# Performance work log

Measured on AMD Instinct MI355X. Metric: run time of the kernel, lower is better.

The kernel has to match this reference:

```python
import jax, jax.numpy as jnp
import numpy as np

H = 256          # hidden_dim
T = 3            # number of agent types (hard-coded in module)
N = 24576        # total agents, contiguous by type
N3 = N // T      # agents per type


def _ln(x, s, b):
    mu = jnp.mean(x, -1, keepdims=True)
    v = jnp.var(x, -1, keepdims=True)
    return (x - mu) * jax.lax.rsqrt(v + 1e-5) * s + b


def setup_inputs() -> dict:
    key = jax.random.key(0)
    ks = jax.random.split(key, 20)
    def p(i, shape, scale=0.02):
        return jax.random.normal(ks[i], shape, jnp.float32) * scale
    inp = {}
    inp['agent_x'] = p(0, (N, H), 1.0)
    inp['lane_x'] = p(1, (N, H), 1.0)
    inp['poly_x'] = p(2, (N, H), 1.0)
    inp['l2a_src'] = jax.random.randint(ks[3], (N,), 0, N)
    inp['g2a_src'] = jax.random.randint(ks[4], (N,), 0, N)
    # other_src[s, d] = src agent of type s for dst agent d (types contiguous)
    inp['other_src'] = jax.random.randint(ks[5], (T, N), 0, N3) + (jnp.arange(T) * N3)[:, None]
    # per-agent-type params
    inp['self_W'] = p(6, (T, H, H)); inp['self_b'] = jnp.zeros((T, H))
    inp['out_W'] = p(7, (T, 4 * H, H)); inp['out_b'] = jnp.zeros((T, H))
    inp['ffn_ln_s'] = jnp.ones((T, H)); inp['ffn_ln_b'] = jnp.zeros((T, H))
    inp['ffn_w1'] = p(8, (T, H, 4 * H)); inp['ffn_b1'] = jnp.zeros((T, 4 * H))
    inp['ffn_w2'] = p(9, (T, 4 * H, H)); inp['ffn_b2'] = jnp.zeros((T, H))
    inp['ffn_w3'] = p(10, (T, H, 4 * H)); inp['ffn_b3'] = jnp.zeros((T, 4 * H))
    # shared edge MLPs (prenorm: LN -> w1 -> relu -> w2)
    inp['l2a_ln_s'] = jnp.ones((3 * H,)); inp['l2a_ln_b'] = jnp.zeros((3 * H,))
    inp['l2a_w1'] = p(11, (3 * H, 4 * H)); inp['l2a_b1'] = jnp.zeros((4 * H,))
    inp['l2a_w2'] = p(12, (4 * H, H)); inp['l2a_b2'] = jnp.zeros((H,))
    inp['g2a_ln_s'] = jnp.ones((2 * H,)); inp['g2a_ln_b'] = jnp.zeros((2 * H,))
    inp['g2a_w1'] = p(13, (2 * H, 4 * H)); inp['g2a_b1'] = jnp.zeros((4 * H,))
    inp['g2a_w2'] = p(14, (4 * H, H)); inp['g2a_b2'] = jnp.zeros((H,))
    # per-src-agent-type 'other' MLPs
    inp['oth_ln_s'] = jnp.ones((T, 3 * H)); inp['oth_ln_b'] = jnp.zeros((T, 3 * H))
    inp['oth_w1'] = p(15, (T, 3 * H, 4 * H)); inp['oth_b1'] = jnp.zeros((T, 4 * H))
    inp['oth_w2'] = p(16, (T, 4 * H, H)); inp['oth_b2'] = jnp.zeros((T, H))
    return inp


def reference(agent_x, lane_x, poly_x, self_W, self_b, out_W, out_b,
              ffn_ln_s, ffn_ln_b, ffn_w1, ffn_b1, ffn_w2, ffn_b2, ffn_w3, ffn_b3,
              l2a_ln_s, l2a_ln_b, l2a_w1, l2a_b1, l2a_w2, l2a_b2,
              g2a_ln_s, g2a_ln_b, g2a_w1, g2a_b1, g2a_w2, g2a_b2,
              oth_ln_s, oth_ln_b, oth_w1, oth_b1, oth_w2, oth_b2,
              l2a_src, g2a_src, other_src):
    x = agent_x.reshape(T, N3, H)                      # agents grouped by type
    # self branch: Linear + ReLU per type
    self_out = jax.nn.relu(jnp.einsum('tnh,thk->tnk', x, self_W) + self_b[:, None, :])
    # l2a edge MLP: cat([lane, agent, lane]) -> prenorm MLP (shared weights)
    lane_feat = lane_x[l2a_src].reshape(T, N3, H)
    l2a_in = jnp.concatenate([lane_feat, x, lane_feat], -1)      # [T,N3,3H]
    l2a_out = jax.nn.relu(_ln(l2a_in, l2a_ln_s, l2a_ln_b) @ l2a_w1 + l2a_b1) @ l2a_w2 + l2a_b2
    # g2a edge MLP: cat([polygon, agent])
    poly_feat = poly_x[g2a_src].reshape(T, N3, H)
    g2a_in = jnp.concatenate([poly_feat, x], -1)                 # [T,N3,2H]
    g2a_out = jax.nn.relu(_ln(g2a_in, g2a_ln_s, g2a_ln_b) @ g2a_w1 + g2a_b1) @ g2a_w2 + g2a_b2
    # agent-other-agent: per source-agent-type MLP, then aggregate over src types
    src_feat = agent_x[other_src].reshape(T, T, N3, H)           # [src_t, dst_t, N3, H]
    xb = jnp.broadcast_to(x[None], (T, T, N3, H))
    oth_in = jnp.concatenate([src_feat, xb, src_feat], -1)       # [s,t,n,3H]
    oth_n = _ln(oth_in, oth_ln_s[:, None, None, :], oth_ln_b[:, None, None, :])
    oth_h = jax.nn.relu(jnp.einsum('stnd,sdm->stnm', oth_n, oth_w1) + oth_b1[:, None, None, :])
    oth_out = jnp.einsum('stnm,smh->stnh', oth_h, oth_w2) + oth_b2[:, None, None, :]
    other_agg = oth_out.sum(0)                                   # [T,N3,H]
    # fuse 4 branches -> out_fc -> PositionwiseFeedForward -> residual
    fused = jnp.concatenate([self_out, l2a_out, g2a_out, other_agg], -1)  # [T,N3,4H]
    out = jnp.einsum('tnd,tdh->tnh', fused, out_W) + out_b[:, None, :]
    y = _ln(out, ffn_ln_s[:, None, :], ffn_ln_b[:, None, :])
    g = jax.nn.silu(jnp.einsum('tnh,thm->tnm', y, ffn_w1) + ffn_b1[:, None, :])
    u = jnp.einsum('tnh,thm->tnm', y, ffn_w3) + ffn_b3[:, None, :]
    out = out + jnp.einsum('tnm,tmh->tnh', g * u, ffn_w2) + ffn_b2[:, None, :]
    return (out + x).reshape(N, H)
```

## Files before the change

### kernel.cpp

```cpp
#include <hip/hip_runtime.h>
#include <hip/hip_bf16.h>

typedef __hip_bfloat16 bf16;
typedef __bf16 v8bf __attribute__((ext_vector_type(8)));
typedef float f32x4 __attribute__((ext_vector_type(4)));

#define N_AG 24576
#define N3 8192

struct __align__(8) bf4 { bf16 x, y, z, w; };
__device__ __forceinline__ bf4 mk4(float a, float b, float c, float d) {
  bf4 r{__float2bfloat16(a), __float2bfloat16(b), __float2bfloat16(c), __float2bfloat16(d)};
  return r;
}

enum {
  EPI_RELU_BIAS = 0,
  EPI_BIAS      = 1,
  EPI_ACC_INIT  = 2,
  EPI_ACC_ADD   = 3,
  EPI_FINAL     = 4,
  EPI_SILU      = 5,
  EPI_MUL       = 6
};

__device__ __forceinline__ void gl_lds16(const bf16* g, short* l) {
  __builtin_amdgcn_global_load_lds(
      (const __attribute__((address_space(1))) unsigned int*)g,
      (__attribute__((address_space(3))) unsigned int*)l, 16, 0, 0);
}

template<int EPI>
__device__ __forceinline__
void gemm_body(const bf16* __restrict__ A, int lda,
               const bf16* __restrict__ Bt, int ldb,
               const float* __restrict__ bias,
               float* __restrict__ accbuf,
               bf16* __restrict__ Cout, int ldc,
               const float* __restrict__ resid,
               float* __restrict__ CoutF,
               const bf16* __restrict__ gin,
               int K, int Nc, int row0, int col0)
{
  __shared__ __align__(16) short As[128 * 32];
  __shared__ __align__(16) short Bs[128 * 32];

  const int tid  = threadIdx.x;
  const int lane = tid & 63;
  const int w    = tid >> 6;
  const int quad = lane >> 4;
  const int l15  = lane & 15;

  f32x4 acc[4][4];
  const f32x4 zero = {0.f, 0.f, 0.f, 0.f};
#pragma unroll
  for (int i = 0; i < 4; ++i)
#pragma unroll
    for (int j = 0; j < 4; ++j) acc[i][j] = zero;

  const int srow = (w << 5) + (lane >> 2);
  const int ss   = ((lane >> 2) & 3) ^ ((lane >> 4) & 1);
  const int sc   = ((lane & 3) ^ ss) << 3;
  const bf16* aG = A  + (long)(row0 + srow) * lda + sc;
  const bf16* bG = Bt + (long)(col0 + srow) * ldb + sc;
  short* AsW = As + w * 1024;
  short* BsW = Bs + w * 1024;

  const int wr = (w >> 1) * 64;
  const int wc = (w & 1) * 64;
  const int fs = (l15 & 3) ^ ((l15 >> 2) & 1);

  for (int k0 = 0; k0 < K; k0 += 32) {
    gl_lds16(aG + k0,                  AsW);
    gl_lds16(aG + k0 + (long)16 * lda, AsW + 512);
    gl_lds16(bG + k0,                  BsW);
    gl_lds16(bG + k0 + (long)16 * ldb, BsW + 512);
    __syncthreads();

    const int pc = (quad ^ fs) * 8;
    v8bf af[4], bfm[4];
#pragma unroll
    for (int i = 0; i < 4; ++i) {
      af[i]  = *(const v8bf*)&As[(wr + i * 16 + l15) * 32 + pc];
      bfm[i] = *(const v8bf*)&Bs[(wc + i * 16 + l15) * 32 + pc];
    }
#pragma unroll
    for (int i = 0; i < 4; ++i)
#pragma unroll
      for (int j = 0; j < 4; ++j)
        acc[i][j] = __builtin_amdgcn_mfma_f32_16x16x32_bf16(af[i], bfm[j], acc[i][j], 0, 0, 0);
    __syncthreads();
  }

#pragma unroll
  for (int ct = 0; ct < 4; ++ct) {
    const int col = col0 + wc + ct * 16 + l15;
    const float bv = bias ? bias[col] : 0.f;
#pragma unroll
    for (int rt = 0; rt < 4; ++rt) {
#pragma unroll
      for (int i = 0; i < 4; ++i) {
        const int row = row0 + wr + rt * 16 + quad * 4 + i;
        float v = acc[rt][ct][i] + bv;
        if constexpr (EPI == EPI_RELU_BIAS) {
          Cout[(long)row * ldc + col] = __float2bfloat16(v > 0.f ? v : 0.f);
        } else if constexpr (EPI == EPI_BIAS) {
          Cout[(long)row * ldc + col] = __float2bfloat16(v);
        } else if constexpr (EPI == EPI_ACC_INIT) {
          accbuf[(long)row * Nc + col] = v;
        } else if constexpr (EPI == EPI_ACC_ADD) {
          accbuf[(long)row * Nc + col] += v;
        } else if constexpr (EPI == EPI_FINAL) {
          CoutF[(long)row * ldc + col] =
              accbuf[(long)row * Nc + col] + v + resid[(long)row * ldc + col];
        } else if constexpr (EPI == EPI_SILU) {
          Cout[(long)row * ldc + col] = __float2bfloat16(v / (1.f + expf(-v)));
        } else {
          const float g = __bfloat162float(gin[(long)row * ldc + col]);
          Cout[(long)row * ldc + col] = __float2bfloat16(v * g);
        }
      }
    }
  }
}

template<int EPI>
__global__ __launch_bounds__(256)
void gemm_k(const bf16* __restrict__ A, int lda,
            const bf16* __restrict__ Bt, int ldb, long bTs,
            const float* __restrict__ bias, long biasTs,
            float* __restrict__ accbuf,
            bf16* __restrict__ Cout, int ldc,
            const float* __restrict__ resid,
            float* __restrict__ CoutF,
            const bf16* __restrict__ gin,
            int K, int Nc)
{
  const int row0 = blockIdx.x * 128;
  const int col0 = blockIdx.y * 128;
  const int t    = row0 >> 13;
  gemm_body<EPI>(A, lda, Bt + (long)t * bTs, ldb,
                 bias ? bias + (long)t * biasTs : nullptr,
                 accbuf, Cout, ldc, resid, CoutF, gin, K, Nc, row0, col0);
}

__global__ __launch_bounds__(256)
void w2m_k(const bf16* __restrict__ outwT, const bf16* __restrict__ w2c,
           bf16* __restrict__ w2m)
{
  const int z = blockIdx.z, b = z / 3, t = z % 3;
  const int j = (b == 0) ? 1 : (b == 1) ? 2 : 3;
  gemm_body<EPI_BIAS>(outwT + (long)t * 262144 + j * 256, 1024,
                      w2c + (long)b * 262144, 256,
                      nullptr, nullptr, w2m + (long)z * 262144, 1024,
                      nullptr, nullptr, nullptr, 256, 1024,
                      blockIdx.x * 128, blockIdx.y * 128);
}

__global__ __launch_bounds__(256)
void transpose_k(const float* __restrict__ src, bf16* __restrict__ dst,
                 int K, int Nc, long sB, long dB)
{
  __shared__ bf16 tile[32][33];
  const int b = blockIdx.z;
  const float* s = src + (long)b * sB;
  bf16* d = dst + (long)b * dB;
  const int kb = blockIdx.y * 32, nb = blockIdx.x * 32;
  const int tx = threadIdx.x & 31, ty = threadIdx.x >> 5;
#pragma unroll
  for (int i = 0; i < 32; i += 8)
    tile[ty + i][tx] = __float2bfloat16(s[(long)(kb + ty + i) * Nc + nb + tx]);
  __syncthreads();
#pragma unroll
  for (int i = 0; i < 32; i += 8)
    d[(long)(nb + ty + i) * K + kb + tx] = tile[tx][ty + i];
}

struct FoldP { const float* w1[5]; const float* ls[5]; };
__global__ __launch_bounds__(256)
void fold_w1_k(FoldP p, bf16* __restrict__ dst)
{
  __shared__ float tile[32][33];
  const int z = blockIdx.z;
  const float* w1 = p.w1[z];
  const float* ls = p.ls[z];
  bf16* d = dst + (long)z * 524288;
  const int n0 = blockIdx.x * 32, i0 = blockIdx.y * 32;
  const int tx = threadIdx.x & 31, ty = threadIdx.x >> 5;
  const bool three = (z != 1) && (i0 < 256);
#pragma unroll
  for (int ii = 0; ii < 32; ii += 8) {
    const int row = i0 + ty + ii;
    float v = ls[row] * w1[(long)row * 1024 + n0 + tx];
    if (three) v += ls[row + 512] * w1[(long)(row + 512) * 1024 + n0 + tx];
    tile[ty + ii][tx] = v;
  }
  __syncthreads();
#pragma unroll
  for (int ii = 0; ii < 32; ii += 8)
    d[(long)(n0 + ty + ii) * 512 + i0 + tx] = __float2bfloat16(tile[tx][ty + ii]);
}

struct BInitP { const float* b1[5]; };
__global__ __launch_bounds__(256)
void binit_k(BInitP p, float* __restrict__ B1F,
             const float* __restrict__ out_b, float* __restrict__ TB)
{
  const int i = blockIdx.x * 256 + threadIdx.x;
  if (i < 5120)            B1F[i] = p.b1[i >> 10][i & 1023];
  else if (i < 5120 + 768) TB[i - 5120] = out_b[i - 5120];
}

struct B1P { const float* w1[5]; const float* lb[5]; int kin[5]; };
__global__ __launch_bounds__(256)
void b1f_add_k(B1P p, float* __restrict__ dst)
{
  const int z   = blockIdx.x;
  const int kin = p.kin[z];
  const int kpb = (kin + 31) >> 5;
  const int k0  = blockIdx.y * kpb;
  const int k1  = min(k0 + kpb, kin);
  const float* w1 = p.w1[z];
  const float* lb = p.lb[z];
  const int n = threadIdx.x;
  float a0 = 0.f, a1 = 0.f, a2 = 0.f, a3 = 0.f;
  for (int k = k0; k < k1; ++k) {
    const float l = lb[k];
    const float* row = w1 + (long)k * 1024;
    a0 += l * row[n];       a1 += l * row[n + 256];
    a2 += l * row[n + 512]; a3 += l * row[n + 768];
  }
  float* d = dst + z * 1024 + n;
  atomicAdd(d, a0);       atomicAdd(d + 256, a1);
  atomicAdd(d + 512, a2); atomicAdd(d + 768, a3);
}

__global__ __launch_bounds__(256)
void tbias_add_k(const float* __restrict__ outW,
                 const float* __restrict__ l2a_b2, const float* __restrict__ g2a_b2,
                 const float* __restrict__ oth_b2, float* __restrict__ dst)
{
  const int t = blockIdx.x, h = threadIdx.x;
  const float* W = outW + (long)t * 262144;
  const int c0 = blockIdx.y * 32;
  float acc = 0.f;
  for (int c = c0; c < c0 + 32; ++c) {
    acc += l2a_b2[c] * W[(256 + c) * 256 + h];
    acc += g2a_b2[c] * W[(512 + c) * 256 + h];
    acc += (oth_b2[c] + oth_b2[256 + c] + oth_b2[512 + c]) * W[(768 + c) * 256 + h];
  }
  atomicAdd(&dst[t * 256 + h], acc);
}

__global__ __launch_bounds__(256)
void cast_k(const float* __restrict__ src, bf16* __restrict__ dst)
{
  const long i = (long)blockIdx.x * 256 + threadIdx.x;
  const float4 v = ((const float4*)src)[i];
  ((bf4*)dst)[i] = mk4(v.x, v.y, v.z, v.w);
}

__device__ __forceinline__ void wave_reduce2(float& s, float& q) {
#pragma unroll
  for (int off = 32; off > 0; off >>= 1) {
    s += __shfl_xor(s, off, 64);
    q += __shfl_xor(q, off, 64);
  }
}

template<int THREE>
__global__ __launch_bounds__(256)
void ln_norm_k(const float* __restrict__ feat, const float* __restrict__ x,
               const int* __restrict__ srcIdx, bf16* __restrict__ out)
{
  const int w = threadIdx.x >> 6, lane = threadIdx.x & 63;
  const int r = blockIdx.x * 4 + w;
  const int src = srcIdx[r];
  const float4 f4 = ((const float4*)(feat + (long)src * 256))[lane];
  const float4 x4 = ((const float4*)(x + (long)r * 256))[lane];
  const float fw = THREE ? 2.f : 1.f;
  float s = fw * (f4.x + f4.y + f4.z + f4.w) + (x4.x + x4.y + x4.z + x4.w);
  float q = fw * (f4.x * f4.x + f4.y * f4.y + f4.z * f4.z + f4.w * f4.w) +
            (x4.x * x4.x + x4.y * x4.y + x4.z * x4.z + x4.w * x4.w);
  wave_reduce2(s, q);
  const float rD  = THREE ? (1.f / 768.f) : (1.f / 512.f);
  const float mu  = s * rD;
  const float var = q * rD - mu * mu;
  const float inv = rsqrtf(var + 1e-5f);
  bf4* o = (bf4*)(out + (long)r * 512);
  o[lane]      = mk4((f4.x - mu) * inv, (f4.y - mu) * inv,
                     (f4.z - mu) * inv, (f4.w - mu) * inv);
  o[64 + lane] = mk4((x4.x - mu) * inv, (x4.y - mu) * inv,
                     (x4.z - mu) * inv, (x4.w - mu) * inv);
}

__global__ __launch_bounds__(256)
void ln_cat3_k(const float* __restrict__ feat, const float* __restrict__ x,
               const int* __restrict__ srcIdx,
               const float* __restrict__ ls, const float* __restrict__ lb,
               bf16* __restrict__ out)
{
  const int w = threadIdx.x >> 6, lane = threadIdx.x & 63;
  const int r = blockIdx.x * 4 + w;
  const int src = srcIdx[r];
  const float4 f4 = ((const float4*)(feat + (long)src * 256))[lane];
  const float4 x4 = ((const float4*)(x + (long)r * 256))[lane];
  float s = 2.f * (f4.x + f4.y + f4.z + f4.w) + (x4.x + x4.y + x4.z + x4.w);
  float q = 2.f * (f4.x * f4.x + f4.y * f4.y + f4.z * f4.z + f4.w * f4.w) +
            (x4.x * x4.x + x4.y * x4.y + x4.z * x4.z + x4.w * x4.w);
  wave_reduce2(s, q);
  const float mu  = s * (1.f / 768.f);
  const float var = q * (1.f / 768.f) - mu * mu;
  const float inv = rsqrtf(var + 1e-5f);
  const float4 s0 = ((const float4*)ls)[lane],         b0 = ((const float4*)lb)[lane];
  const float4 s1 = ((const float4*)(ls + 256))[lane], b1 = ((const float4*)(lb + 256))[lane];
  const float4 s2 = ((const float4*)(ls + 512))[lane], b2 = ((const float4*)(lb + 512))[lane];
  bf4* o = (bf4*)(out + (long)r * 768);
  o[lane] = mk4((f4.x - mu) * inv * s0.x + b0.x, (f4.y - mu) * inv * s0.y + b0.y,
                (f4.z - mu) * inv * s0.z + b0.z, (f4.w - mu) * inv * s0.w + b0.w);
  o[64 + lane] = mk4((x4.x - mu) * inv * s1.x + b1.x, (x4.y - mu) * inv * s1.y + b1.y,
                     (x4.z - mu) * inv * s1.z + b1.z, (x4.w - mu) * inv * s1.w + b1.w);
  o[128 + lane] = mk4((f4.x - mu) * inv * s2.x + b2.x, (f4.y - mu) * inv * s2.y + b2.y,
                      (f4.z - mu) * inv * s2.z + b2.z, (f4.w - mu) * inv * s2.w + b2.w);
}

__global__ __launch_bounds__(256)
void ln_cat2_k(const float* __restrict__ feat, const float* __restrict__ x,
               const int* __restrict__ srcIdx,
               const float* __restrict__ ls, const float* __restrict__ lb,
               bf16* __restrict__ out)
{
  const int w = threadIdx.x >> 6, lane = threadIdx.x & 63;
  const int r = blockIdx.x * 4 + w;
  const int src = srcIdx[r];
  const float4 f4 = ((const float4*)(feat + (long)src * 256))[lane];
  const float4 x4 = ((const float4*)(x + (long)r * 256))[lane];
  float s = (f4.x + f4.y + f4.z + f4.w) + (x4.x + x4.y + x4.z + x4.w);
  float q = (f4.x * f4.x + f4.y * f4.y + f4.z * f4.z + f4.w * f4.w) +
            (x4.x * x4.x + x4.y * x4.y + x4.z * x4.z + x4.w * x4.w);
  wave_reduce2(s, q);
  const float mu  = s * (1.f / 512.f);
  const float var = q * (1.f / 512.f) - mu * mu;
  const float inv = rsqrtf(var + 1e-5f);
  const float4 s0 = ((const float4*)ls)[lane],         b0 = ((const float4*)lb)[lane];
  const float4 s1 = ((const float4*)(ls + 256))[lane], b1 = ((const float4*)(lb + 256))[lane];
  bf4* o = (bf4*)(out + (long)r * 512);
  o[lane] = mk4((f4.x - mu) * inv * s0.x + b0.x, (f4.y - mu) * inv * s0.y + b0.y,
                (f4.z - mu) * inv * s0.z + b0.z, (f4.w - mu) * inv * s0.w + b0.w);
  o[64 + lane] = mk4((x4.x - mu) * inv * s1.x + b1.x, (x4.y - mu) * inv * s1.y + b1.y,
                     (x4.z - mu) * inv * s1.z + b1.z, (x4.w - mu) * inv * s1.w + b1.w);
}

__global__ __launch_bounds__(256)
void ln_ffn_k(const float* __restrict__ ob, const float* __restrict__ ls,
              const float* __restrict__ lb, bf16* __restrict__ y, long lsStride)
{
  const int w = threadIdx.x >> 6, lane = threadIdx.x & 63;
  const int r = blockIdx.x * 4 + w;
  const long po = (long)(r >> 13) * lsStride;
  const float4 v4 = ((const float4*)(ob + (long)r * 256))[lane];
  float s = v4.x + v4.y + v4.z + v4.w;
  float q = v4.x * v4.x + v4.y * v4.y + v4.z * v4.z + v4.w * v4.w;
  wave_reduce2(s, q);
  const float mu  = s * (1.f / 256.f);
  const float var = q * (1.f / 256.f) - mu * mu;
  const float inv = rsqrtf(var + 1e-5f);
  const float4 s0 = ((const float4*)(ls + po))[lane];
  const float4 b0 = ((const float4*)(lb + po))[lane];
  ((bf4*)(y + (long)r * 256))[lane] =
      mk4((v4.x - mu) * inv * s0.x + b0.x, (v4.y - mu) * inv * s0.y + b0.y,
          (v4.z - mu) * inv * s0.z + b0.z, (v4.w - mu) * inv * s0.w + b0.w);
}

__global__ __launch_bounds__(256)
void silu_mul_k(bf16* __restrict__ g, const bf16* __restrict__ u)
{
  const long i = (long)blockIdx.x * 256 + threadIdx.x;
  const bf4 g4 = ((const bf4*)g)[i];
  const bf4 u4 = ((const bf4*)u)[i];
  float a = __bfloat162float(g4.x), b = __bfloat162float(g4.y);
  float c = __bfloat162float(g4.z), d = __bfloat162float(g4.w);
  a = a / (1.f + expf(-a)) * __bfloat162float(u4.x);
  b = b / (1.f + expf(-b)) * __bfloat162float(u4.y);
  c = c / (1.f + expf(-c)) * __bfloat162float(u4.z);
  d = d / (1.f + expf(-d)) * __bfloat162float(u4.w);
  ((bf4*)g)[i] = mk4(a, b, c, d);
}

__global__ __launch_bounds__(256)
void fill_k(float* __restrict__ p, int n)
{
  const int i = blockIdx.x * 256 + threadIdx.x;
  if (i < n) p[i] = 2.0f;
}

extern "C" void kernel_launch(void* const* d_in, const int* in_sizes, int n_in,
                              void* d_out, int out_size, void* d_ws, size_t ws_size,
                              hipStream_t stream)
{
  const float* agent_x  = (const float*)d_in[0];
  const float* lane_x   = (const float*)d_in[1];
  const float* poly_x   = (const float*)d_in[2];
  const int*   l2a_src  = (const int*)d_in[3];
  const int*   g2a_src  = (const int*)d_in[4];
  const int*   other_src= (const int*)d_in[5];
  const float* self_W   = (const float*)d_in[6];
  const float* self_b   = (const float*)d_in[7];
  const float* out_W    = (const float*)d_in[8];
  const float* out_b    = (const float*)d_in[9];
  const float* ffn_ln_s = (const float*)d_in[10];
  const float* ffn_ln_b = (const float*)d_in[11];
  const float* ffn_w1   = (const float*)d_in[12];
  const float* ffn_b1   = (const float*)d_in[13];
  const float* ffn_w2   = (const float*)d_in[14];
  const float* ffn_b2   = (const float*)d_in[15];
  const float* ffn_w3   = (const float*)d_in[16];
  const float* ffn_b3   = (const float*)d_in[17];
  const float* l2a_ln_s = (const float*)d_in[18];
  const float* l2a_ln_b = (const float*)d_in[19];
  const float* l2a_w1   = (const float*)d_in[20];
  const float* l2a_b1   = (const float*)d_in[21];
  const float* l2a_w2   = (const float*)d_in[22];
  const float* l2a_b2   = (const float*)d_in[23];
  const float* g2a_ln_s = (const float*)d_in[24];
  const float* g2a_ln_b = (const float*)d_in[25];
  const float* g2a_w1   = (const float*)d_in[26];
  const float* g2a_b1   = (const float*)d_in[27];
  const float* g2a_w2   = (const float*)d_in[28];
  const float* g2a_b2   = (const float*)d_in[29];
  const float* oth_ln_s = (const float*)d_in[30];
  const float* oth_ln_b = (const float*)d_in[31];
  const float* oth_w1   = (const float*)d_in[32];
  const float* oth_b1   = (const float*)d_in[33];
  const float* oth_w2   = (const float*)d_in[34];
  const float* oth_b2   = (const float*)d_in[35];

  float* outp = (float*)d_out;
  const dim3 B256(256);

  const size_t TIER_A = 135684096;
  const size_t TIER_C = 12058624;

  if (ws_size >= TIER_A) {
    char* base = (char*)d_ws;
    bf16* wT = (bf16*)base;
    const long SELF_WT = 0,       OUT_WT  = 196608,  FFN_W1T = 983040;
    const long FFN_W3T = 1769472, FFN_W2T = 2555904;
    const long W2C = 3342336,     W1F     = 4653056, W2M     = 7274496;
    float* B1F  = (float*)(base + 22413312L);
    float* TB   = (float*)(base + 22433792L);
    bf16*  nbuf = (bf16*)(base + 22437888L);
    bf16*  h1   = (bf16*)(base + 47603712L);
    float* oF   = (float*)(base + 97935360L);
    bf16*  ybuf = (bf16*)(base + 123101184L);
    bf16*  xbf  = h1;

    auto TRB = [&](const float* s, long dOff, int K, int Nc, long sB, long dB, int b) {
      transpose_k<<<dim3(Nc / 32, K / 32, b), B256, 0, stream>>>(s, wT + dOff, K, Nc, sB, dB);
    };
    TRB(self_W, SELF_WT, 256, 256,  65536, 65536, 3);
    TRB(out_W,  OUT_WT,  1024, 256, 262144, 262144, 3);
    TRB(ffn_w1, FFN_W1T, 256, 1024, 262144, 262144, 3);
    TRB(ffn_w3, FFN_W3T, 256, 1024, 262144, 262144, 3);
    TRB(ffn_w2, FFN_W2T, 1024, 256, 262144, 262144, 3);
    cast_k<<<256, B256, 0, stream>>>(l2a_w2, wT + W2C);
    cast_k<<<256, B256, 0, stream>>>(g2a_w2, wT + W2C + 262144);
    cast_k<<<768, B256, 0, stream>>>(oth_w2, wT + W2C + 524288);

    FoldP fp = {{l2a_w1, g2a_w1, oth_w1, oth_w1 + 786432, oth_w1 + 1572864},
                {l2a_ln_s, g2a_ln_s, oth_ln_s, oth_ln_s + 768, oth_ln_s + 1536}};
    fold_w1_k<<<dim3(32, 16, 5), B256, 0, stream>>>(fp, wT + W1F);

    BInitP ip = {{l2a_b1, g2a_b1, oth_b1, oth_b1 + 1024, oth_b1 + 2048}};
    binit_k<<<23, B256, 0, stream>>>(ip, B1F, out_b, TB);
    B1P bp = {{l2a_w1, g2a_w1, oth_w1, oth_w1 + 786432, oth_w1 + 1572864},
              {l2a_ln_b, g2a_ln_b, oth_ln_b, oth_ln_b + 768, oth_ln_b + 1536},
              {768, 512, 768, 768, 768}};
    b1f_add_k<<<dim3(5, 32), B256, 0, stream>>>(bp, B1F);
    tbias_add_k<<<dim3(3, 8), B256, 0, stream>>>(out_W, l2a_b2, g2a_b2, oth_b2, TB);
    w2m_k<<<dim3(2, 8, 15), B256, 0, stream>>>(wT + OUT_WT, wT + W2C, wT + W2M);

    const dim3 Gw1(N_AG / 128, 8), Gw2(N_AG / 128, 2);

    cast_k<<<N_AG / 4, B256, 0, stream>>>(agent_x, xbf);
    gemm_k<EPI_RELU_BIAS><<<Gw2, B256, 0, stream>>>(
        xbf, 256, wT + SELF_WT, 256, 65536, self_b, 256,
        nullptr, ybuf, 256, nullptr, nullptr, nullptr, 256, 256);
    gemm_k<EPI_ACC_INIT><<<Gw2, B256, 0, stream>>>(
        ybuf, 256, wT + OUT_WT, 1024, 262144, TB, 256,
        oF, nullptr, 0, nullptr, nullptr, nullptr, 256, 256);

    for (int b = 0; b < 5; ++b) {
      const int* src = (b == 0) ? l2a_src : (b == 1) ? g2a_src
                                          : other_src + (long)(b - 2) * N_AG;
      const float* feat = (b == 0) ? lane_x : (b == 1) ? poly_x : agent_x;
      if (b == 1) ln_norm_k<0><<<N_AG / 4, B256, 0, stream>>>(feat, agent_x, src, nbuf);
      else        ln_norm_k<1><<<N_AG / 4, B256, 0, stream>>>(feat, agent_x, src, nbuf);
      gemm_k<EPI_RELU_BIAS><<<Gw1, B256, 0, stream>>>(
          nbuf, 512, wT + W1F + (long)b * 524288, 512, 0, B1F + b * 1024, 0,
          nullptr, h1, 1024, nullptr, nullptr, nullptr, 512, 1024);
      gemm_k<EPI_ACC_ADD><<<Gw2, B256, 0, stream>>>(
          h1, 1024, wT + W2M + (long)b * 786432, 1024, 262144, nullptr, 0,
          oF, nullptr, 0, nullptr, nullptr, nullptr, 1024, 256);
    }

    ln_ffn_k<<<N_AG / 4, B256, 0, stream>>>(oF, ffn_ln_s, ffn_ln_b, ybuf, 256);
    gemm_k<EPI_SILU><<<Gw1, B256, 0, stream>>>(
        ybuf, 256, wT + FFN_W1T, 256, 262144, ffn_b1, 1024,
        nullptr, h1, 1024, nullptr, nullptr, nullptr, 256, 1024);
    gemm_k<EPI_MUL><<<Gw1, B256, 0, stream>>>(
        ybuf, 256, wT + FFN_W3T, 256, 262144, ffn_b3, 1024,
        nullptr, h1, 1024, nullptr, nullptr, h1, 256, 1024);
    gemm_k<EPI_FINAL><<<Gw2, B256, 0, stream>>>(
        h1, 1024, wT + FFN_W2T, 1024, 262144, ffn_b2, 256,
        oF, nullptr, 256, agent_x, outp, nullptr, 1024, 256);
    return;
  }

  if (ws_size < TIER_C) {
    fill_k<<<(out_size + 255) / 256, B256, 0, stream>>>(outp, out_size);
    return;
  }

  const int CH = 2048;
  char* base = (char*)d_ws;
  bf16*  wt     = (bf16*)base;
  bf16*  nbuf   = (bf16*)(base + 1572864L);
  bf16*  bbuf   = (bf16*)(base + 4718592L);
  bf16*  h1     = (bf16*)(base + 5767168L);
  float* outF32 = (float*)(base + 9961472L);
  bf16*  ybuf   = (bf16*)(base + 524288L);
  bf16*  xbf    = h1;
  bf16*  g_pre  = h1;
  bf16*  u_pre  = nbuf;

  const dim3 Gw1(CH / 128, 8), Gw2(CH / 128, 2);
  auto TR = [&](const float* s, int K, int Nc) {
    transpose_k<<<dim3(Nc / 32, K / 32), B256, 0, stream>>>(s, wt, K, Nc, 0, 0);
  };

  for (int t = 0; t < 3; ++t) {
    for (int c = 0; c < N3 / CH; ++c) {
      const long r0 = (long)t * N3 + (long)c * CH;
      const float* xC   = agent_x + r0 * 256;
      float*       outC = outp + r0 * 256;

      cast_k<<<CH / 4, B256, 0, stream>>>(xC, xbf);
      TR(self_W + (long)t * 65536, 256, 256);
      gemm_k<EPI_RELU_BIAS><<<Gw2, B256, 0, stream>>>(
          xbf, 256, wt, 256, 0, self_b + t * 256, 0, nullptr, bbuf, 256,
          nullptr, nullptr, nullptr, 256, 256);
      TR(out_W + (long)t * 262144 + 0 * 65536, 256, 256);
      gemm_k<EPI_ACC_INIT><<<Gw2, B256, 0, stream>>>(
          bbuf, 256, wt, 256, 0, out_b + t * 256, 0, outF32, nullptr, 0,
          nullptr, nullptr, nullptr, 256, 256);

      ln_cat3_k<<<CH / 4, B256, 0, stream>>>(lane_x, xC, l2a_src + r0,
                                             l2a_ln_s, l2a_ln_b, nbuf);
      TR(l2a_w1, 768, 1024);
      gemm_k<EPI_RELU_BIAS><<<Gw1, B256, 0, stream>>>(
          nbuf, 768, wt, 768, 0, l2a_b1, 0, nullptr, h1, 1024,
          nullptr, nullptr, nullptr, 768, 1024);
      TR(l2a_w2, 1024, 256);
      gemm_k<EPI_BIAS><<<Gw2, B256, 0, stream>>>(
          h1, 1024, wt, 1024, 0, l2a_b2, 0, nullptr, bbuf, 256,
          nullptr, nullptr, nullptr, 1024, 256);
      TR(out_W + (long)t * 262144 + 1 * 65536, 256, 256);
      gemm_k<EPI_ACC_ADD><<<Gw2, B256, 0, stream>>>(
          bbuf, 256, wt, 256, 0, nullptr, 0, outF32, nullptr, 0,
          nullptr, nullptr, nullptr, 256, 256);

      ln_cat2_k<<<CH / 4, B256, 0, stream>>>(poly_x, xC, g2a_src + r0,
                                             g2a_ln_s, g2a_ln_b, nbuf);
      TR(g2a_w1, 512, 1024);
      gemm_k<EPI_RELU_BIAS><<<Gw1, B256, 0, stream>>>(
          nbuf, 512, wt, 512, 0, g2a_b1, 0, nullptr, h1, 1024,
          nullptr, nullptr, nullptr, 512, 1024);
      TR(g2a_w2, 1024, 256);
      gemm_k<EPI_BIAS><<<Gw2, B256, 0, stream>>>(
          h1, 1024, wt, 1024, 0, g2a_b2, 0, nullptr, bbuf, 256,
          nullptr, nullptr, nullptr, 1024, 256);
      TR(out_W + (long)t * 262144 + 2 * 65536, 256, 256);
      gemm_k<EPI_ACC_ADD><<<Gw2, B256, 0, stream>>>(
          bbuf, 256, wt, 256, 0, nullptr, 0, outF32, nullptr, 0,
          nullptr, nullptr, nullptr, 256, 256);

      for (int s = 0; s < 3; ++s) {
        ln_cat3_k<<<CH / 4, B256, 0, stream>>>(
            agent_x, xC, other_src + (long)s * N_AG + r0,
            oth_ln_s + s * 768, oth_ln_b + s * 768, nbuf);
        TR(oth_w1 + (long)s * 786432, 768, 1024);
        gemm_k<EPI_RELU_BIAS><<<Gw1, B256, 0, stream>>>(
            nbuf, 768, wt, 768, 0, oth_b1 + s * 1024, 0, nullptr, h1, 1024,
            nullptr, nullptr, nullptr, 768, 1024);
        TR(oth_w2 + (long)s * 262144, 1024, 256);
        gemm_k<EPI_BIAS><<<Gw2, B256, 0, stream>>>(
            h1, 1024, wt, 1024, 0, oth_b2 + s * 256, 0, nullptr, bbuf, 256,
            nullptr, nullptr, nullptr, 1024, 256);
        TR(out_W + (long)t * 262144 + 3 * 65536, 256, 256);
        gemm_k<EPI_ACC_ADD><<<Gw2, B256, 0, stream>>>(
            bbuf, 256, wt, 256, 0, nullptr, 0, outF32, nullptr, 0,
            nullptr, nullptr, nullptr, 256, 256);
      }

      ln_ffn_k<<<CH / 4, B256, 0, stream>>>(outF32, ffn_ln_s + t * 256,
                                            ffn_ln_b + t * 256, ybuf, 0);
      TR(ffn_w1 + (long)t * 262144, 256, 1024);
      gemm_k<EPI_BIAS><<<Gw1, B256, 0, stream>>>(
          ybuf, 256, wt, 256, 0, ffn_b1 + t * 1024, 0, nullptr, g_pre, 1024,
          nullptr, nullptr, nullptr, 256, 1024);
      TR(ffn_w3 + (long)t * 262144, 256, 1024);
      gemm_k<EPI_BIAS><<<Gw1, B256, 0, stream>>>(
          ybuf, 256, wt, 256, 0, ffn_b3 + t * 1024, 0, nullptr, u_pre, 1024,
          nullptr, nullptr, nullptr, 256, 1024);
      silu_mul_k<<<CH, B256, 0, stream>>>(g_pre, u_pre);
      TR(ffn_w2 + (long)t * 262144, 1024, 256);
      gemm_k<EPI_FINAL><<<Gw2, B256, 0, stream>>>(
          g_pre, 1024, wt, 1024, 0, ffn_b2 + t * 256, 0, outF32, nullptr, 256,
          xC, outC, nullptr, 1024, 256);
    }
  }
}
```

Before: 911.0 us.

## Double-buffer GEMM LDS tiles and fuse FFN w1/w3 GEMMs into one GLU GEMM

```diff
diff --git a/kernel.cpp b/kernel.cpp
--- a/kernel.cpp
+++ b/kernel.cpp
@@ -21,7 +21,8 @@
   EPI_ACC_ADD   = 3,
   EPI_FINAL     = 4,
   EPI_SILU      = 5,
-  EPI_MUL       = 6
+  EPI_MUL       = 6,
+  EPI_GLU       = 7
 };
 
 __device__ __forceinline__ void gl_lds16(const bf16* g, short* l) {
@@ -42,8 +43,8 @@
                const bf16* __restrict__ gin,
                int K, int Nc, int row0, int col0)
 {
-  __shared__ __align__(16) short As[128 * 32];
-  __shared__ __align__(16) short Bs[128 * 32];
+  __shared__ __align__(16) short As[2][128 * 32];
+  __shared__ __align__(16) short Bs[2][128 * 32];
 
   const int tid  = threadIdx.x;
   const int lane = tid & 63;
@@ -63,26 +64,37 @@
   const int sc   = ((lane & 3) ^ ss) << 3;
   const bf16* aG = A  + (long)(row0 + srow) * lda + sc;
   const bf16* bG = Bt + (long)(col0 + srow) * ldb + sc;
-  short* AsW = As + w * 1024;
-  short* BsW = Bs + w * 1024;
+  const int ldsOff = w * 1024;
 
   const int wr = (w >> 1) * 64;
   const int wc = (w & 1) * 64;
   const int fs = (l15 & 3) ^ ((l15 >> 2) & 1);
 
+  gl_lds16(aG,                  As[0] + ldsOff);
+  gl_lds16(aG + (long)16 * lda, As[0] + ldsOff + 512);
+  gl_lds16(bG,                  Bs[0] + ldsOff);
+  gl_lds16(bG + (long)16 * ldb, Bs[0] + ldsOff + 512);
+  __syncthreads();
+
+  int cur = 0;
   for (int k0 = 0; k0 < K; k0 += 32) {
-    gl_lds16(aG + k0,                  AsW);
-    gl_lds16(aG + k0 + (long)16 * lda, AsW + 512);
-    gl_lds16(bG + k0,                  BsW);
-    gl_lds16(bG + k0 + (long)16 * ldb, BsW + 512);
-    __syncthreads();
-
+    const int nk = k0 + 32;
+    if (nk < K) {
+      short* An = As[cur ^ 1] + ldsOff;
+      short* Bn = Bs[cur ^ 1] + ldsOff;
+      gl_lds16(aG + nk,                  An);
+      gl_lds16(aG + nk + (long)16 * lda, An + 512);
+      gl_lds16(bG + nk,                  Bn);
+      gl_lds16(bG + nk + (long)16 * ldb, Bn + 512);
+    }
+    const short* Ac = As[cur];
+    const short* Bc = Bs[cur];
     const int pc = (quad ^ fs) * 8;
     v8bf af[4], bfm[4];
 #pragma unroll
     for (int i = 0; i < 4; ++i) {
-      af[i]  = *(const v8bf*)&As[(wr + i * 16 + l15) * 32 + pc];
-      bfm[i] = *(const v8bf*)&Bs[(wc + i * 16 + l15) * 32 + pc];
+      af[i]  = *(const v8bf*)&Ac[(wr + i * 16 + l15) * 32 + pc];
+      bfm[i] = *(const v8bf*)&Bc[(wc + i * 16 + l15) * 32 + pc];
     }
 #pragma unroll
     for (int i = 0; i < 4; ++i)
@@ -90,34 +102,56 @@
       for (int j = 0; j < 4; ++j)
         acc[i][j] = __builtin_amdgcn_mfma_f32_16x16x32_bf16(af[i], bfm[j], acc[i][j], 0, 0, 0);
     __syncthreads();
-  }
-
-#pragma unroll
-  for (int ct = 0; ct < 4; ++ct) {
-    const int col = col0 + wc + ct * 16 + l15;
-    const float bv = bias ? bias[col] : 0.f;
-#pragma unroll
-    for (int rt = 0; rt < 4; ++rt) {
-#pragma unroll
-      for (int i = 0; i < 4; ++i) {
-        const int row = row0 + wr + rt * 16 + quad * 4 + i;
-        float v = acc[rt][ct][i] + bv;
-        if constexpr (EPI == EPI_RELU_BIAS) {
-          Cout[(long)row * ldc + col] = __float2bfloat16(v > 0.f ? v : 0.f);
-        } else if constexpr (EPI == EPI_BIAS) {
-          Cout[(long)row * ldc + col] = __float2bfloat16(v);
-        } else if constexpr (EPI == EPI_ACC_INIT) {
-          accbuf[(long)row * Nc + col] = v;
-        } else if constexpr (EPI == EPI_ACC_ADD) {
-          accbuf[(long)row * Nc + col] += v;
-        } else if constexpr (EPI == EPI_FINAL) {
-          CoutF[(long)row * ldc + col] =
-              accbuf[(long)row * Nc + col] + v + resid[(long)row * ldc + col];
-        } else if constexpr (EPI == EPI_SILU) {
-          Cout[(long)row * ldc + col] = __float2bfloat16(v / (1.f + expf(-v)));
-        } else {
-          const float g = __bfloat162float(gin[(long)row * ldc + col]);
-          Cout[(long)row * ldc + col] = __float2bfloat16(v * g);
+    cur ^= 1;
+  }
+
+  if constexpr (EPI == EPI_GLU) {
+#pragma unroll
+    for (int ct = 0; ct < 4; ct += 2) {
+      const int colg = col0 + wc + ct * 16 + l15;
+      const int hcol = ((colg >> 5) << 4) + (colg & 15);
+      const float bg = bias[colg];
+      const float bu = bias[colg + 16];
+#pragma unroll
+      for (int rt = 0; rt < 4; ++rt) {
+#pragma unroll
+        for (int i = 0; i < 4; ++i) {
+          const int row = row0 + wr + rt * 16 + quad * 4 + i;
+          const float vg = acc[rt][ct][i] + bg;
+          const float vu = acc[rt][ct + 1][i] + bu;
+          Cout[(long)row * ldc + hcol] =
+              __float2bfloat16(vg / (1.f + expf(-vg)) * vu);
+        }
+      }
+    }
+  } else {
+#pragma unroll
+    for (int ct = 0; ct < 4; ++ct) {
+      const int col = col0 + wc + ct * 16 + l15;
+      const float bv = bias ? bias[col] : 0.f;
+#pragma unroll
+      for (int rt = 0; rt < 4; ++rt) {
+#pragma unroll
+        for (int i = 0; i < 4; ++i) {
+          const int row = row0 + wr + rt * 16 + quad * 4 + i;
+          float v = acc[rt][ct][i] + bv;
+          if constexpr (EPI == EPI_RELU_BIAS) {
+            Cout[(long)row * ldc + col] = __float2bfloat16(v > 0.f ? v : 0.f);
+          } else if constexpr (EPI == EPI_BIAS) {
+            Cout[(long)row * ldc + col] = __float2bfloat16(v);
+          } else if constexpr (EPI == EPI_ACC_INIT) {
+            accbuf[(long)row * Nc + col] = v;
+          } else if constexpr (EPI == EPI_ACC_ADD) {
+            accbuf[(long)row * Nc + col] += v;
+          } else if constexpr (EPI == EPI_FINAL) {
+            CoutF[(long)row * ldc + col] =
+                accbuf[(long)row * Nc + col] + v + resid[(long)row * ldc + col];
+          } else if constexpr (EPI == EPI_SILU) {
+            Cout[(long)row * ldc + col] = __float2bfloat16(v / (1.f + expf(-v)));
+          } else {
+            const float g = __bfloat162float(gin[(long)row * ldc + col]);
+            Cout[(long)row * ldc + col] = __float2bfloat16(v * g);
+          }
         }
       }
     }
@@ -176,6 +210,27 @@
     d[(long)(nb + ty + i) * K + kb + tx] = tile[tx][ty + i];
 }
 
+__global__ __launch_bounds__(256)
+void transpose13_k(const float* __restrict__ w1, const float* __restrict__ w3,
+                   bf16* __restrict__ dst)
+{
+  __shared__ bf16 tile[32][33];
+  const int t  = blockIdx.z;
+  const int n0 = blockIdx.x * 32;
+  const int k0 = blockIdx.y * 32;
+  const int gi = n0 >> 5;
+  const int tx = threadIdx.x & 31, ty = threadIdx.x >> 5;
+  const float* src = ((tx & 16) ? w3 : w1) + (long)t * 262144;
+  const int c = 16 * gi + (tx & 15);
+#pragma unroll
+  for (int i = 0; i < 32; i += 8)
+    tile[ty + i][tx] = __float2bfloat16(src[(long)(k0 + ty + i) * 1024 + c]);
+  __syncthreads();
+#pragma unroll
+  for (int i = 0; i < 32; i += 8)
+    dst[((long)t * 2048 + n0 + ty + i) * 256 + k0 + tx] = tile[tx][ty + i];
+}
+
 struct FoldP { const float* w1[5]; const float* ls[5]; };
 __global__ __launch_bounds__(256)
 void fold_w1_k(FoldP p, bf16* __restrict__ dst)
@@ -201,14 +256,23 @@
     d[(long)(n0 + ty + ii) * 512 + i0 + tx] = __float2bfloat16(tile[tx][ty + ii]);
 }
 
-struct BInitP { const float* b1[5]; };
+struct BInitP { const float* b1[5]; const float* fb1; const float* fb3; };
 __global__ __launch_bounds__(256)
 void binit_k(BInitP p, float* __restrict__ B1F,
-             const float* __restrict__ out_b, float* __restrict__ TB)
+             const float* __restrict__ out_b, float* __restrict__ TB,
+             float* __restrict__ B13)
 {
   const int i = blockIdx.x * 256 + threadIdx.x;
-  if (i < 5120)            B1F[i] = p.b1[i >> 10][i & 1023];
-  else if (i < 5120 + 768) TB[i - 5120] = out_b[i - 5120];
+  if (i < 5120) {
+    B1F[i] = p.b1[i >> 10][i & 1023];
+  } else if (i < 5888) {
+    TB[i - 5120] = out_b[i - 5120];
+  } else if (i < 12032) {
+    const int idx = i - 5888;
+    const int t = idx >> 11, n = idx & 2047;
+    const int c = ((n >> 5) << 4) | (n & 15);
+    B13[idx] = (n & 16) ? p.fb3[t * 1024 + c] : p.fb1[t * 1024 + c];
+  }
 }
 
 struct B1P { const float* w1[5]; const float* lb[5]; int kin[5]; };
@@ -438,21 +502,22 @@
   float* outp = (float*)d_out;
   const dim3 B256(256);
 
-  const size_t TIER_A = 135684096;
+  const size_t TIER_A = 135707648;
   const size_t TIER_C = 12058624;
 
   if (ws_size >= TIER_A) {
     char* base = (char*)d_ws;
     bf16* wT = (bf16*)base;
-    const long SELF_WT = 0,       OUT_WT  = 196608,  FFN_W1T = 983040;
-    const long FFN_W3T = 1769472, FFN_W2T = 2555904;
-    const long W2C = 3342336,     W1F     = 4653056, W2M     = 7274496;
+    const long SELF_WT = 0,       OUT_WT  = 196608,  FFN_W13T = 983040;
+    const long FFN_W2T = 2555904;
+    const long W2C = 3342336,     W1F     = 4653056, W2M      = 7274496;
     float* B1F  = (float*)(base + 22413312L);
     float* TB   = (float*)(base + 22433792L);
-    bf16*  nbuf = (bf16*)(base + 22437888L);
-    bf16*  h1   = (bf16*)(base + 47603712L);
-    float* oF   = (float*)(base + 97935360L);
-    bf16*  ybuf = (bf16*)(base + 123101184L);
+    float* B13  = (float*)(base + 22436864L);
+    bf16*  nbuf = (bf16*)(base + 22461440L);
+    bf16*  h1   = (bf16*)(base + 47627264L);
+    float* oF   = (float*)(base + 97958912L);
+    bf16*  ybuf = (bf16*)(base + 123124736L);
     bf16*  xbf  = h1;
 
     auto TRB = [&](const float* s, long dOff, int K, int Nc, long sB, long dB, int b) {
@@ -460,9 +525,8 @@
     };
     TRB(self_W, SELF_WT, 256, 256,  65536, 65536, 3);
     TRB(out_W,  OUT_WT,  1024, 256, 262144, 262144, 3);
-    TRB(ffn_w1, FFN_W1T, 256, 1024, 262144, 262144, 3);
-    TRB(ffn_w3, FFN_W3T, 256, 1024, 262144, 262144, 3);
     TRB(ffn_w2, FFN_W2T, 1024, 256, 262144, 262144, 3);
+    transpose13_k<<<dim3(64, 8, 3), B256, 0, stream>>>(ffn_w1, ffn_w3, wT + FFN_W13T);
     cast_k<<<256, B256, 0, stream>>>(l2a_w2, wT + W2C);
     cast_k<<<256, B256, 0, stream>>>(g2a_w2, wT + W2C + 262144);
     cast_k<<<768, B256, 0, stream>>>(oth_w2, wT + W2C + 524288);
@@ -471,8 +535,8 @@
                 {l2a_ln_s, g2a_ln_s, oth_ln_s, oth_ln_s + 768, oth_ln_s + 1536}};
     fold_w1_k<<<dim3(32, 16, 5), B256, 0, stream>>>(fp, wT + W1F);
 
-    BInitP ip = {{l2a_b1, g2a_b1, oth_b1, oth_b1 + 1024, oth_b1 + 2048}};
-    binit_k<<<23, B256, 0, stream>>>(ip, B1F, out_b, TB);
+    BInitP ip = {{l2a_b1, g2a_b1, oth_b1, oth_b1 + 1024, oth_b1 + 2048}, ffn_b1, ffn_b3};
+    binit_k<<<47, B256, 0, stream>>>(ip, B1F, out_b, TB, B13);
     B1P bp = {{l2a_w1, g2a_w1, oth_w1, oth_w1 + 786432, oth_w1 + 1572864},
               {l2a_ln_b, g2a_ln_b, oth_ln_b, oth_ln_b + 768, oth_ln_b + 1536},
               {768, 512, 768, 768, 768}};
@@ -480,7 +544,7 @@
     tbias_add_k<<<dim3(3, 8), B256, 0, stream>>>(out_W, l2a_b2, g2a_b2, oth_b2, TB);
     w2m_k<<<dim3(2, 8, 15), B256, 0, stream>>>(wT + OUT_WT, wT + W2C, wT + W2M);
 
-    const dim3 Gw1(N_AG / 128, 8), Gw2(N_AG / 128, 2);
+    const dim3 Gw1(N_AG / 128, 8), Gw2(N_AG / 128, 2), Gglu(N_AG / 128, 16);
 
     cast_k<<<N_AG / 4, B256, 0, stream>>>(agent_x, xbf);
     gemm_k<EPI_RELU_BIAS><<<Gw2, B256, 0, stream>>>(
@@ -505,12 +569,9 @@
     }
 
     ln_ffn_k<<<N_AG / 4, B256, 0, stream>>>(oF, ffn_ln_s, ffn_ln_b, ybuf, 256);
-    gemm_k<EPI_SILU><<<Gw1, B256, 0, stream>>>(
-        ybuf, 256, wT + FFN_W1T, 256, 262144, ffn_b1, 1024,
-        nullptr, h1, 1024, nullptr, nullptr, nullptr, 256, 1024);
-    gemm_k<EPI_MUL><<<Gw1, B256, 0, stream>>>(
-        ybuf, 256, wT + FFN_W3T, 256, 262144, ffn_b3, 1024,
-        nullptr, h1, 1024, nullptr, nullptr, h1, 256, 1024);
+    gemm_k<EPI_GLU><<<Gglu, B256, 0, stream>>>(
+        ybuf, 256, wT + FFN_W13T, 256, 524288, B13, 2048,
+        nullptr, h1, 1024, nullptr, nullptr, nullptr, 256, 2048);
     gemm_k<EPI_FINAL><<<Gw2, B256, 0, stream>>>(
         h1, 1024, wT + FFN_W2T, 1024, 262144, ffn_b2, 256,
         oF, nullptr, 256, agent_x, outp, nullptr, 1024, 256);
```

New measurement: 844.1 us. 7.3% less time.
